# Optimization experiments

Hardware: AMD Instinct MI355X
Metric: run time of the kernel (lower is better)

## Reference

```python
import jax, jax.numpy as jnp
import numpy as np


def setup_inputs() -> dict:
    key = jax.random.key(0)
    ks = jax.random.split(key, 8)
    B, S, Ta, D = 64, 512, 8, 768
    return {
        "memory": jax.random.normal(ks[0], (B, S, D), dtype=jnp.float32),
        "aspect_states": jax.random.normal(ks[1], (B, Ta, D), dtype=jnp.float32),
        "input_ids": jnp.ones((B, S), dtype=jnp.int64),
        "input_t_ids": jnp.ones((B, Ta), dtype=jnp.int64),
        "W1": jax.random.normal(ks[2], (3 * D, D), dtype=jnp.float32) * 0.02,
        "b1": jnp.zeros((D,), dtype=jnp.float32),
        "w2": jax.random.normal(ks[3], (D,), dtype=jnp.float32) * 0.02,
        "Wm": jax.random.normal(ks[4], (D, D), dtype=jnp.float32) * 0.02,
        "bm": jnp.zeros((D,), dtype=jnp.float32),
        "Wd": jax.random.normal(ks[5], (D, 3), dtype=jnp.float32) * 0.02,
        "bd": jnp.zeros((3,), dtype=jnp.float32),
    }


def reference(memory, aspect_states, input_ids, input_t_ids, W1, b1, w2, Wm, bm, Wd, bd):
    B, S, D = memory.shape
    memory_len = jnp.sum(input_ids != 0, axis=-1)          # [B]
    aspect_len = jnp.sum(input_t_ids != 0, axis=-1)        # [B]

    # v_a: mean-pooled aspect representation  [B, D]
    v_a = jnp.sum(aspect_states, axis=1) / aspect_len.astype(memory.dtype)[:, None]
    # v_s: mean-pooled sentence representation [B, D]
    v_s = jnp.sum(memory, axis=1) / memory_len.astype(memory.dtype)[:, None]

    # locationed_memory: memory[i, idx] *= 1 - idx/memory_len[i] for idx < memory_len[i]
    idx = jnp.arange(S, dtype=memory.dtype)                 # [S]
    mlen = memory_len.astype(memory.dtype)[:, None]         # [B, 1]
    loc = jnp.where(idx[None, :] < mlen, 1.0 - idx[None, :] / mlen, 1.0)  # [B, S]
    memory = memory * loc[:, :, None]

    # chunked linear1/linear2 scorer, vectorized:
    # c_t = w2 . tanh(W1 @ [m_t ; v_a ; v_s] + b1)
    W1_m, W1_a, W1_s = W1[:D], W1[D:2 * D], W1[2 * D:]
    ctx = v_a @ W1_a + v_s @ W1_s + b1                      # [B, D]
    h = jnp.tanh(jnp.einsum("bsd,de->bse", memory, W1_m) + ctx[:, None, :])
    scores = h @ w2                                         # [B, S]
    alpha = jax.nn.softmax(scores, axis=1)

    v_ts = jnp.einsum("bsd,bs->bd", memory, alpha)          # [B, D]
    v_ns = v_ts + v_s
    v_ms = jnp.tanh(v_ns @ Wm + bm)
    logits = v_ms @ Wd + bd                                 # [B, 3]
    return logits
```

## Files before the change

### kernel.cpp

```cpp
#include <hip/hip_runtime.h>
#include <hip/hip_bf16.h>


#define NB 64
#define NS 512
#define ND 768
#define NTA 8

typedef __attribute__((ext_vector_type(8))) __bf16 bf16x8;
typedef __attribute__((ext_vector_type(4))) float f32x4;

#define OFF_SCORES 0u
#define OFF_VS 131072u
#define OFF_VTS 327680u
#define OFF_CTX 524288u
#define OFF_U 720896u
#define ZERO_BYTES 917504u
#define OFF_VA 917504u
#define OFF_LENS 1245184u
#define OFF_W1MT 1246208u
#define OFF_MP 2425856u

__device__ __forceinline__ float fast_tanh(float x) {
  x = fminf(fmaxf(x, -15.f), 15.f);
  float t = __expf(2.f * x);
  return __fdividef(t - 1.f, t + 1.f);
}

__device__ __forceinline__ unsigned bfpack2(float a, float b) {
  unsigned ua = __float_as_uint(a), ub = __float_as_uint(b);
  ua = (ua + 0x7FFFu + ((ua >> 16) & 1u)) >> 16;
  ub = (ub + 0x7FFFu + ((ub >> 16) & 1u)) >> 16;
  return ua | (ub << 16);
}

__device__ __forceinline__ unsigned short bf16b(float f) {
  unsigned u = __float_as_uint(f);
  u = (u + 0x7FFFu + ((u >> 16) & 1u)) >> 16;
  return (unsigned short)u;
}

__device__ __forceinline__ void async_copy16(const void* g, void* l) {
  __builtin_amdgcn_global_load_lds(
      (const __attribute__((address_space(1))) void*)g,
      (__attribute__((address_space(3))) void*)l, 16, 0, 0);
}

__global__ __launch_bounds__(256) void k_pre(const float* __restrict__ W1,
                                             unsigned short* __restrict__ w1mt,
                                             const int* __restrict__ ids,
                                             const int* __restrict__ tids,
                                             const float* __restrict__ aspect,
                                             float* __restrict__ v_a,
                                             float* __restrict__ lens,
                                             char* __restrict__ zws) {
  int bid = blockIdx.x, tid = threadIdx.x;
  if (bid < 576) {
    __shared__ float tile[32][33];
    int bx = bid % 24, by = bid / 24;
    int tx = tid & 31, ty = tid >> 5;
    for (int j = 0; j < 32; j += 8)
      tile[ty + j][tx] = W1[(size_t)(by * 32 + ty + j) * ND + bx * 32 + tx];
    __syncthreads();
    for (int j = 0; j < 32; j += 8)
      w1mt[(size_t)(bx * 32 + ty + j) * ND + by * 32 + tx] = bf16b(tile[tx][ty + j]);
  } else if (bid < 640) {
    int b = bid - 576;
    __shared__ int red[256];
    __shared__ float sh_inva;
    int cnt = 0;
    for (int j = tid; j < NS; j += 256) cnt += (ids[b * NS + j] != 0);
    red[tid] = cnt;
    __syncthreads();
    for (int s = 128; s > 0; s >>= 1) {
      if (tid < s) red[tid] += red[tid + s];
      __syncthreads();
    }
    if (tid == 0) {
      int mlen = red[0];
      int acnt = 0;
      for (int t = 0; t < NTA; ++t) acnt += (tids[b * NTA + t] != 0);
      lens[b] = (float)mlen;
      lens[64 + b] = 1.0f / (float)mlen;
      float inva = 1.0f / (float)acnt;
      lens[128 + b] = inva;
      sh_inva = inva;
    }
    __syncthreads();
    float inva = sh_inva;
    for (int j = tid; j < ND; j += 256) {
      float s = 0.f;
      for (int t = 0; t < NTA; ++t) s += aspect[((size_t)b * NTA + t) * ND + j];
      v_a[b * ND + j] = s * inva;
    }
  } else {
    uint4 z = {0u, 0u, 0u, 0u};
    *(uint4*)(zws + (size_t)(bid - 640) * 4096 + tid * 16) = z;
  }
}

__global__ __launch_bounds__(192) void k_vs_mprime(const float* __restrict__ memory,
                                                   const float* __restrict__ lens,
                                                   float* __restrict__ v_s,
                                                   unsigned short* __restrict__ mp) {
  int sc = blockIdx.x, b = blockIdx.y, tid = threadIdx.x;
  int d0 = tid * 4;
  float inv_mlen = lens[64 + b];
  float mlenf = lens[b];
  float s0 = 0, s1 = 0, s2 = 0, s3 = 0;
  for (int s = 0; s < 32; ++s) {
    int srow = sc * 32 + s;
    size_t row = (size_t)b * NS + srow;
    const float4 v = *(const float4*)(memory + row * ND + d0);
    s0 += v.x; s1 += v.y; s2 += v.z; s3 += v.w;
    float fs = (float)srow;
    float loc = (fs < mlenf) ? 1.0f - fs * inv_mlen : 1.0f;
    uint2 pk;
    pk.x = bfpack2(v.x * loc, v.y * loc);
    pk.y = bfpack2(v.z * loc, v.w * loc);
    *(uint2*)(mp + row * ND + d0) = pk;
  }
  float* p = v_s + b * ND + d0;
  atomicAdd(p + 0, s0 * inv_mlen);
  atomicAdd(p + 1, s1 * inv_mlen);
  atomicAdd(p + 2, s2 * inv_mlen);
  atomicAdd(p + 3, s3 * inv_mlen);
}

__global__ __launch_bounds__(256) void k_ctx(const float* __restrict__ W1,
                                             const float* __restrict__ v_a,
                                             const float* __restrict__ v_s,
                                             float* __restrict__ ctx) {
  int et = blockIdx.x, bt = blockIdx.y, dc = blockIdx.z, tid = threadIdx.x;
  __shared__ float vbuf[8][192];
  int b0 = bt * 8;
  for (int l = tid; l < 8 * 192; l += 256) {
    int bb = l / 192, jj = l % 192;
    int k = dc * 192 + jj;
    vbuf[bb][jj] = (k < ND) ? v_a[(b0 + bb) * ND + k] : v_s[(b0 + bb) * ND + (k - ND)];
  }
  __syncthreads();
  int e = et * 256 + tid;
  const float* Wk = W1 + (size_t)(ND + dc * 192) * ND + e;
  float acc[8] = {0.f, 0.f, 0.f, 0.f, 0.f, 0.f, 0.f, 0.f};
#pragma unroll 4
  for (int j = 0; j < 192; ++j) {
    float w = Wk[(size_t)j * ND];
#pragma unroll
    for (int bb = 0; bb < 8; ++bb) acc[bb] += vbuf[bb][j] * w;
  }
#pragma unroll
  for (int bb = 0; bb < 8; ++bb) atomicAdd(&ctx[(b0 + bb) * ND + e], acc[bb]);
}

__global__ __launch_bounds__(256) void k_gemm_scores(const unsigned short* __restrict__ mp,
                                                     const unsigned short* __restrict__ w1mt,
                                                     const float* __restrict__ ctx,
                                                     const float* __restrict__ b1,
                                                     const float* __restrict__ w2,
                                                     float* __restrict__ scores) {
  __shared__ char lds[32768];
  char* ldsA = lds;
  char* ldsB = lds + 16384;
  const int tid = threadIdx.x;
  const int wave = tid >> 6, lane = tid & 63;
  const int bid = blockIdx.x;
  const int xcd = bid & 7, j = bid >> 3;
  const int et = j % 6;
  const int rt = xcd * 32 + j / 6;
  const int row0 = rt * 128, n0 = et * 128;
  const int b = row0 >> 9;
  const int wm = wave & 1, wn = wave >> 1;

  const int lrow = lane >> 3;
  const int qlog = (lane & 7) ^ lrow;
  const char* Abase = (const char*)mp + (size_t)(row0 + lrow) * (ND * 2) + qlog * 16;
  const char* Bbase = (const char*)w1mt + (size_t)(n0 + lrow) * (ND * 2) + qlog * 16;

  f32x4 acc[4][4];
#pragma unroll
  for (int i = 0; i < 4; ++i)
#pragma unroll
    for (int t = 0; t < 4; ++t) acc[i][t] = (f32x4){0.f, 0.f, 0.f, 0.f};

  const int q2 = lane >> 4, c = lane & 15;
  int offA0[4], offB0[4];
#pragma unroll
  for (int i = 0; i < 4; ++i) {
    int ml = wm * 64 + i * 16 + c;
    offA0[i] = ml * 128 + ((q2 ^ (ml & 7)) * 16);
    int nl = wn * 64 + i * 16 + c;
    offB0[i] = nl * 128 + ((q2 ^ (nl & 7)) * 16);
  }

  for (int kb = 0; kb < ND * 2; kb += 128) {
#pragma unroll
    for (int i = 0; i < 4; ++i) {
      int g = wave * 4 + i;
      async_copy16(Abase + (size_t)g * 8 * (ND * 2) + kb, ldsA + g * 1024);
      async_copy16(Bbase + (size_t)g * 8 * (ND * 2) + kb, ldsB + g * 1024);
    }
    __syncthreads();
#pragma unroll
    for (int kk = 0; kk < 2; ++kk) {
      const int x = kk * 64;
      bf16x8 bfrag[4];
#pragma unroll
      for (int t = 0; t < 4; ++t) bfrag[t] = *(const bf16x8*)(ldsB + (offB0[t] ^ x));
#pragma unroll
      for (int i = 0; i < 4; ++i) {
        bf16x8 afrag = *(const bf16x8*)(ldsA + (offA0[i] ^ x));
#pragma unroll
        for (int t = 0; t < 4; ++t)
          acc[i][t] = __builtin_amdgcn_mfma_f32_16x16x32_bf16(afrag, bfrag[t], acc[i][t], 0, 0, 0);
      }
    }
    __syncthreads();
  }

  float ctxv[4], w2v[4];
#pragma unroll
  for (int t = 0; t < 4; ++t) {
    int n = n0 + wn * 64 + t * 16 + c;
    ctxv[t] = ctx[b * ND + n] + b1[n];
    w2v[t] = w2[n];
  }
#pragma unroll
  for (int i = 0; i < 4; ++i) {
#pragma unroll
    for (int r = 0; r < 4; ++r) {
      float s = 0.f;
#pragma unroll
      for (int t = 0; t < 4; ++t) s += fast_tanh(acc[i][t][r] + ctxv[t]) * w2v[t];
      s += __shfl_xor(s, 1, 64);
      s += __shfl_xor(s, 2, 64);
      s += __shfl_xor(s, 4, 64);
      s += __shfl_xor(s, 8, 64);
      if (c == 0) atomicAdd(&scores[row0 + wm * 64 + i * 16 + q2 * 4 + r], s);
    }
  }
}

__global__ __launch_bounds__(192) void k_vts_sm(const unsigned short* __restrict__ mp,
                                                const float* __restrict__ scores,
                                                float* __restrict__ v_ts) {
  int sc = blockIdx.x, b = blockIdx.y, tid = threadIdx.x;
  int wid = tid >> 6, lane = tid & 63;
  __shared__ float sm[3], ss[3];
  __shared__ float al[32];
  float v[3];
#pragma unroll
  for (int k = 0; k < 3; ++k) {
    int j = tid + k * 192;
    v[k] = (j < NS) ? scores[b * NS + j] : -1e30f;
  }
  float m = fmaxf(fmaxf(v[0], v[1]), v[2]);
  for (int off = 1; off < 64; off <<= 1) m = fmaxf(m, __shfl_xor(m, off, 64));
  if (lane == 0) sm[wid] = m;
  __syncthreads();
  float M = fmaxf(fmaxf(sm[0], sm[1]), sm[2]);
  float e = 0.f;
#pragma unroll
  for (int k = 0; k < 3; ++k)
    if (tid + k * 192 < NS) e += __expf(v[k] - M);
  for (int off = 1; off < 64; off <<= 1) e += __shfl_xor(e, off, 64);
  if (lane == 0) ss[wid] = e;
  __syncthreads();
  float invS = 1.0f / (ss[0] + ss[1] + ss[2]);
  if (tid < 32) al[tid] = __expf(scores[b * NS + sc * 32 + tid] - M) * invS;
  __syncthreads();

  int d0 = tid * 4;
  float a0 = 0, a1 = 0, a2 = 0, a3 = 0;
  for (int s = 0; s < 32; ++s) {
    size_t row = (size_t)b * NS + sc * 32 + s;
    uint2 pk = *(const uint2*)(mp + row * ND + d0);
    float a = al[s];
    a0 += a * __uint_as_float(pk.x << 16);
    a1 += a * __uint_as_float(pk.x & 0xFFFF0000u);
    a2 += a * __uint_as_float(pk.y << 16);
    a3 += a * __uint_as_float(pk.y & 0xFFFF0000u);
  }
  float* p = v_ts + b * ND + d0;
  atomicAdd(p + 0, a0);
  atomicAdd(p + 1, a1);
  atomicAdd(p + 2, a2);
  atomicAdd(p + 3, a3);
}

__global__ __launch_bounds__(256) void k_final1(const float* __restrict__ v_ts,
                                                const float* __restrict__ v_s,
                                                const float* __restrict__ Wm,
                                                float* __restrict__ u) {
  int et = blockIdx.x, bt = blockIdx.y, dc = blockIdx.z, tid = threadIdx.x;
  __shared__ float vbuf[8][192];
  int b0 = bt * 8;
  for (int l = tid; l < 8 * 192; l += 256) {
    int bb = l / 192, jj = l % 192;
    int d = dc * 192 + jj;
    vbuf[bb][jj] = v_ts[(b0 + bb) * ND + d] + v_s[(b0 + bb) * ND + d];
  }
  __syncthreads();
  int e = et * 256 + tid;
  const float* Wk = Wm + (size_t)(dc * 192) * ND + e;
  float acc[8] = {0.f, 0.f, 0.f, 0.f, 0.f, 0.f, 0.f, 0.f};
#pragma unroll 4
  for (int j = 0; j < 192; ++j) {
    float w = Wk[(size_t)j * ND];
#pragma unroll
    for (int bb = 0; bb < 8; ++bb) acc[bb] += vbuf[bb][j] * w;
  }
#pragma unroll
  for (int bb = 0; bb < 8; ++bb) atomicAdd(&u[(b0 + bb) * ND + e], acc[bb]);
}

__global__ __launch_bounds__(256) void k_final2(const float* __restrict__ u,
                                                const float* __restrict__ bm,
                                                const float* __restrict__ Wd,
                                                const float* __restrict__ bd,
                                                float* __restrict__ out) {
  int b = blockIdx.x, tid = threadIdx.x;
  int wid = tid >> 6, lane = tid & 63;
  __shared__ float red[4][3];
  float p0 = 0, p1 = 0, p2 = 0;
  for (int e = tid; e < ND; e += 256) {
    float vm = fast_tanh(u[b * ND + e] + bm[e]);
    p0 += vm * Wd[e * 3 + 0];
    p1 += vm * Wd[e * 3 + 1];
    p2 += vm * Wd[e * 3 + 2];
  }
  for (int off = 1; off < 64; off <<= 1) {
    p0 += __shfl_xor(p0, off, 64);
    p1 += __shfl_xor(p1, off, 64);
    p2 += __shfl_xor(p2, off, 64);
  }
  if (lane == 0) { red[wid][0] = p0; red[wid][1] = p1; red[wid][2] = p2; }
  __syncthreads();
  if (tid == 0) {
    out[b * 3 + 0] = red[0][0] + red[1][0] + red[2][0] + red[3][0] + bd[0];
    out[b * 3 + 1] = red[0][1] + red[1][1] + red[2][1] + red[3][1] + bd[1];
    out[b * 3 + 2] = red[0][2] + red[1][2] + red[2][2] + red[3][2] + bd[2];
  }
}

extern "C" void kernel_launch(void* const* d_in, const int* in_sizes, int n_in,
                              void* d_out, int out_size, void* d_ws, size_t ws_size,
                              hipStream_t stream) {
  const float* memory = (const float*)d_in[0];
  const float* aspect = (const float*)d_in[1];
  const int* ids = (const int*)d_in[2];
  const int* tids = (const int*)d_in[3];
  const float* W1 = (const float*)d_in[4];
  const float* b1 = (const float*)d_in[5];
  const float* w2 = (const float*)d_in[6];
  const float* Wm = (const float*)d_in[7];
  const float* bm = (const float*)d_in[8];
  const float* Wd = (const float*)d_in[9];
  const float* bd = (const float*)d_in[10];
  float* out = (float*)d_out;

  char* ws = (char*)d_ws;
  float* scores = (float*)(ws + OFF_SCORES);
  float* v_s = (float*)(ws + OFF_VS);
  float* v_ts = (float*)(ws + OFF_VTS);
  float* ctx = (float*)(ws + OFF_CTX);
  float* u = (float*)(ws + OFF_U);
  float* v_a = (float*)(ws + OFF_VA);
  float* lens = (float*)(ws + OFF_LENS);
  unsigned short* w1mt = (unsigned short*)(ws + OFF_W1MT);
  unsigned short* mp = (unsigned short*)(ws + OFF_MP);

  k_pre<<<864, 256, 0, stream>>>(W1, w1mt, ids, tids, aspect, v_a, lens, ws);
  k_vs_mprime<<<dim3(16, NB), 192, 0, stream>>>(memory, lens, v_s, mp);
  k_ctx<<<dim3(3, 8, 8), 256, 0, stream>>>(W1, v_a, v_s, ctx);
  k_gemm_scores<<<1536, 256, 0, stream>>>(mp, w1mt, ctx, b1, w2, scores);
  k_vts_sm<<<dim3(16, NB), 192, 0, stream>>>(mp, scores, v_ts);
  k_final1<<<dim3(3, 8, 4), 256, 0, stream>>>(v_ts, v_s, Wm, u);
  k_final2<<<NB, 256, 0, stream>>>(u, bm, Wd, bd, out);
}
```

Before: 324.6 us.

## Fuse all stages into one persistent cooperative kernel with grid syncs

Replaces seven separate kernel launches with a single cooperative persistent kernel that runs each former stage in a grid-stride loop, separated by grid-wide barriers. The aim is to remove per-launch overhead and the gaps between dependent kernels. The grid is sized from the occupancy query, capped at 1024 blocks. Fixed-work stages such as the GEMM now loop over fewer resident blocks, and each grid.sync adds its own barrier cost. The old multi-kernel path is kept as a fallback if the cooperative launch fails.

```diff
diff --git a/kernel.cpp b/kernel.cpp
--- a/kernel.cpp
+++ b/kernel.cpp
@@ -1,5 +1,8 @@
 #include <hip/hip_runtime.h>
 #include <hip/hip_bf16.h>
+#include <hip/hip_cooperative_groups.h>
+
+namespace cg = cooperative_groups;
 
 
 #define NB 64
@@ -44,6 +47,291 @@
   __builtin_amdgcn_global_load_lds(
       (const __attribute__((address_space(1))) void*)g,
       (__attribute__((address_space(3))) void*)l, 16, 0, 0);
+}
+
+__global__ __launch_bounds__(256, 4) void k_mega(
+    const float* __restrict__ memory, const float* __restrict__ aspect,
+    const int* __restrict__ ids, const int* __restrict__ tids,
+    const float* __restrict__ W1, const float* __restrict__ b1,
+    const float* __restrict__ w2, const float* __restrict__ Wm,
+    const float* __restrict__ bm, const float* __restrict__ Wd,
+    const float* __restrict__ bd, float* __restrict__ out,
+    float* __restrict__ scores, float* __restrict__ v_s,
+    float* __restrict__ v_ts, float* __restrict__ ctx, float* __restrict__ u,
+    float* __restrict__ v_a, float* __restrict__ lens,
+    unsigned short* __restrict__ w1mt, unsigned short* __restrict__ mp,
+    char* __restrict__ zws) {
+  cg::grid_group grid = cg::this_grid();
+  const int bid = blockIdx.x, tid = threadIdx.x;
+  const int nblk = gridDim.x;
+  __shared__ __align__(16) char smem[32768];
+
+  for (int vb = bid; vb < 864; vb += nblk) {
+    if (vb < 576) {
+      float(*tile)[33] = (float(*)[33])smem;
+      int bx = vb % 24, by = vb / 24;
+      int tx = tid & 31, ty = tid >> 5;
+      for (int j = 0; j < 32; j += 8)
+        tile[ty + j][tx] = W1[(size_t)(by * 32 + ty + j) * ND + bx * 32 + tx];
+      __syncthreads();
+      for (int j = 0; j < 32; j += 8)
+        w1mt[(size_t)(bx * 32 + ty + j) * ND + by * 32 + tx] = bf16b(tile[tx][ty + j]);
+    } else if (vb < 640) {
+      int b = vb - 576;
+      int* red = (int*)smem;
+      float* sh_inva = (float*)(smem + 1024);
+      int cnt = 0;
+      for (int j = tid; j < NS; j += 256) cnt += (ids[b * NS + j] != 0);
+      red[tid] = cnt;
+      __syncthreads();
+      for (int s = 128; s > 0; s >>= 1) {
+        if (tid < s) red[tid] += red[tid + s];
+        __syncthreads();
+      }
+      if (tid == 0) {
+        int mlen = red[0];
+        int acnt = 0;
+        for (int t = 0; t < NTA; ++t) acnt += (tids[b * NTA + t] != 0);
+        lens[b] = (float)mlen;
+        lens[64 + b] = 1.0f / (float)mlen;
+        float inva = 1.0f / (float)acnt;
+        lens[128 + b] = inva;
+        *sh_inva = inva;
+      }
+      __syncthreads();
+      float inva = *sh_inva;
+      for (int j = tid; j < ND; j += 256) {
+        float s = 0.f;
+        for (int t = 0; t < NTA; ++t) s += aspect[((size_t)b * NTA + t) * ND + j];
+        v_a[b * ND + j] = s * inva;
+      }
+    } else {
+      uint4 z = {0u, 0u, 0u, 0u};
+      *(uint4*)(zws + (size_t)(vb - 640) * 4096 + tid * 16) = z;
+    }
+    __syncthreads();
+  }
+  grid.sync();
+
+  for (int vb = bid; vb < 1024; vb += nblk) {
+    int b = vb >> 4, sc = vb & 15;
+    if (tid < 192) {
+      int d0 = tid * 4;
+      float inv_mlen = lens[64 + b];
+      float mlenf = lens[b];
+      float s0 = 0, s1 = 0, s2 = 0, s3 = 0;
+      for (int s = 0; s < 32; ++s) {
+        int srow = sc * 32 + s;
+        size_t row = (size_t)b * NS + srow;
+        const float4 v = *(const float4*)(memory + row * ND + d0);
+        s0 += v.x; s1 += v.y; s2 += v.z; s3 += v.w;
+        float fs = (float)srow;
+        float loc = (fs < mlenf) ? 1.0f - fs * inv_mlen : 1.0f;
+        uint2 pk;
+        pk.x = bfpack2(v.x * loc, v.y * loc);
+        pk.y = bfpack2(v.z * loc, v.w * loc);
+        *(uint2*)(mp + row * ND + d0) = pk;
+      }
+      float* p = v_s + b * ND + d0;
+      atomicAdd(p + 0, s0 * inv_mlen);
+      atomicAdd(p + 1, s1 * inv_mlen);
+      atomicAdd(p + 2, s2 * inv_mlen);
+      atomicAdd(p + 3, s3 * inv_mlen);
+    }
+  }
+  grid.sync();
+
+  for (int vb = bid; vb < 768; vb += nblk) {
+    int et = vb >> 8, r = vb & 255;
+    int b = r >> 2, dc = r & 3;
+    float* vbuf = (float*)smem;
+    for (int j = tid; j < 384; j += 256) {
+      int k = dc * 384 + j;
+      vbuf[j] = (k < ND) ? v_a[b * ND + k] : v_s[b * ND + (k - ND)];
+    }
+    __syncthreads();
+    int e = et * 256 + tid;
+    float acc = 0.f;
+    const float* Wk = W1 + (size_t)(ND + dc * 384) * ND + e;
+#pragma unroll 8
+    for (int j = 0; j < 384; ++j) acc += vbuf[j] * Wk[(size_t)j * ND];
+    atomicAdd(&ctx[b * ND + e], acc);
+    __syncthreads();
+  }
+  grid.sync();
+
+  {
+    char* ldsA = smem;
+    char* ldsB = smem + 16384;
+    const int wave = tid >> 6, lane = tid & 63;
+    const int wm = wave & 1, wn = wave >> 1;
+    const int lrow = lane >> 3;
+    const int qlog = (lane & 7) ^ lrow;
+    const int q2 = lane >> 4, c = lane & 15;
+
+    for (int t = bid; t < 1536; t += nblk) {
+      const int xcd = t & 7, jj = t >> 3;
+      const int et = jj % 6;
+      const int rt = xcd * 32 + jj / 6;
+      const int row0 = rt * 128, n0 = et * 128;
+      const int b = row0 >> 9;
+
+      const char* Abase = (const char*)mp + (size_t)(row0 + lrow) * (ND * 2) + qlog * 16;
+      const char* Bbase = (const char*)w1mt + (size_t)(n0 + lrow) * (ND * 2) + qlog * 16;
+
+      f32x4 acc[4][4];
+#pragma unroll
+      for (int i = 0; i < 4; ++i)
+#pragma unroll
+        for (int t2 = 0; t2 < 4; ++t2) acc[i][t2] = (f32x4){0.f, 0.f, 0.f, 0.f};
+
+      int offA0[4], offB0[4];
+#pragma unroll
+      for (int i = 0; i < 4; ++i) {
+        int ml = wm * 64 + i * 16 + c;
+        offA0[i] = ml * 128 + ((q2 ^ (ml & 7)) * 16);
+        int nl = wn * 64 + i * 16 + c;
+        offB0[i] = nl * 128 + ((q2 ^ (nl & 7)) * 16);
+      }
+
+      __syncthreads();
+      for (int kb = 0; kb < ND * 2; kb += 128) {
+#pragma unroll
+        for (int i = 0; i < 4; ++i) {
+          int g = wave * 4 + i;
+          async_copy16(Abase + (size_t)g * 8 * (ND * 2) + kb, ldsA + g * 1024);
+          async_copy16(Bbase + (size_t)g * 8 * (ND * 2) + kb, ldsB + g * 1024);
+        }
+        __syncthreads();
+#pragma unroll
+        for (int kk = 0; kk < 2; ++kk) {
+          const int x = kk * 64;
+          bf16x8 bfrag[4];
+#pragma unroll
+          for (int t2 = 0; t2 < 4; ++t2) bfrag[t2] = *(const bf16x8*)(ldsB + (offB0[t2] ^ x));
+#pragma unroll
+          for (int i = 0; i < 4; ++i) {
+            bf16x8 afrag = *(const bf16x8*)(ldsA + (offA0[i] ^ x));
+#pragma unroll
+            for (int t2 = 0; t2 < 4; ++t2)
+              acc[i][t2] = __builtin_amdgcn_mfma_f32_16x16x32_bf16(afrag, bfrag[t2], acc[i][t2], 0, 0, 0);
+          }
+        }
+        __syncthreads();
+      }
+
+      float ctxv[4], w2v[4];
+#pragma unroll
+      for (int t2 = 0; t2 < 4; ++t2) {
+        int n = n0 + wn * 64 + t2 * 16 + c;
+        ctxv[t2] = ctx[b * ND + n] + b1[n];
+        w2v[t2] = w2[n];
+      }
+#pragma unroll
+      for (int i = 0; i < 4; ++i) {
+#pragma unroll
+        for (int r = 0; r < 4; ++r) {
+          float s = 0.f;
+#pragma unroll
+          for (int t2 = 0; t2 < 4; ++t2) s += fast_tanh(acc[i][t2][r] + ctxv[t2]) * w2v[t2];
+          s += __shfl_xor(s, 1, 64);
+          s += __shfl_xor(s, 2, 64);
+          s += __shfl_xor(s, 4, 64);
+          s += __shfl_xor(s, 8, 64);
+          if (c == 0) atomicAdd(&scores[row0 + wm * 64 + i * 16 + q2 * 4 + r], s);
+        }
+      }
+    }
+  }
+  grid.sync();
+
+  for (int vb = bid; vb < 1024; vb += nblk) {
+    int b = vb >> 4, sc = vb & 15;
+    int wid = tid >> 6, lane = tid & 63;
+    float* sm = (float*)smem;
+    float* ssum = sm + 4;
+    float* al = sm + 8;
+    float v0 = scores[b * NS + tid];
+    float v1 = scores[b * NS + 256 + tid];
+    float m = fmaxf(v0, v1);
+    for (int off = 1; off < 64; off <<= 1) m = fmaxf(m, __shfl_xor(m, off, 64));
+    if (lane == 0) sm[wid] = m;
+    __syncthreads();
+    float M = fmaxf(fmaxf(sm[0], sm[1]), fmaxf(sm[2], sm[3]));
+    float e = __expf(v0 - M) + __expf(v1 - M);
+    for (int off = 1; off < 64; off <<= 1) e += __shfl_xor(e, off, 64);
+    if (lane == 0) ssum[wid] = e;
+    __syncthreads();
+    float invS = 1.0f / (ssum[0] + ssum[1] + ssum[2] + ssum[3]);
+    if (tid < 32) al[tid] = __expf(scores[b * NS + sc * 32 + tid] - M) * invS;
+    __syncthreads();
+
+    if (tid < 192) {
+      int d0 = tid * 4;
+      float a0 = 0, a1 = 0, a2 = 0, a3 = 0;
+      for (int s = 0; s < 32; ++s) {
+        size_t row = (size_t)b * NS + sc * 32 + s;
+        uint2 pk = *(const uint2*)(mp + row * ND + d0);
+        float a = al[s];
+        a0 += a * __uint_as_float(pk.x << 16);
+        a1 += a * __uint_as_float(pk.x & 0xFFFF0000u);
+        a2 += a * __uint_as_float(pk.y << 16);
+        a3 += a * __uint_as_float(pk.y & 0xFFFF0000u);
+      }
+      float* p = v_ts + b * ND + d0;
+      atomicAdd(p + 0, a0);
+      atomicAdd(p + 1, a1);
+      atomicAdd(p + 2, a2);
+      atomicAdd(p + 3, a3);
+    }
+    __syncthreads();
+  }
+  grid.sync();
+
+  for (int vb = bid; vb < 768; vb += nblk) {
+    int et = vb >> 8, r = vb & 255;
+    int b = r >> 2, dc = r & 3;
+    float* vbuf = (float*)smem;
+    for (int j = tid; j < 192; j += 256) {
+      int d = dc * 192 + j;
+      vbuf[j] = v_ts[b * ND + d] + v_s[b * ND + d];
+    }
+    __syncthreads();
+    int e = et * 256 + tid;
+    float acc = 0.f;
+    const float* Wk = Wm + (size_t)(dc * 192) * ND + e;
+#pragma unroll 8
+    for (int j = 0; j < 192; ++j) acc += vbuf[j] * Wk[(size_t)j * ND];
+    atomicAdd(&u[b * ND + e], acc);
+    __syncthreads();
+  }
+  grid.sync();
+
+  for (int vb = bid; vb < NB; vb += nblk) {
+    int b = vb;
+    int wid = tid >> 6, lane = tid & 63;
+    float* red = (float*)smem;
+    float p0 = 0, p1 = 0, p2 = 0;
+    for (int e = tid; e < ND; e += 256) {
+      float vm = fast_tanh(u[b * ND + e] + bm[e]);
+      p0 += vm * Wd[e * 3 + 0];
+      p1 += vm * Wd[e * 3 + 1];
+      p2 += vm * Wd[e * 3 + 2];
+    }
+    for (int off = 1; off < 64; off <<= 1) {
+      p0 += __shfl_xor(p0, off, 64);
+      p1 += __shfl_xor(p1, off, 64);
+      p2 += __shfl_xor(p2, off, 64);
+    }
+    if (lane == 0) { red[wid * 3 + 0] = p0; red[wid * 3 + 1] = p1; red[wid * 3 + 2] = p2; }
+    __syncthreads();
+    if (tid == 0) {
+      out[b * 3 + 0] = red[0] + red[3] + red[6] + red[9] + bd[0];
+      out[b * 3 + 1] = red[1] + red[4] + red[7] + red[10] + bd[1];
+      out[b * 3 + 2] = red[2] + red[5] + red[8] + red[11] + bd[2];
+    }
+    __syncthreads();
+  }
 }
 
 __global__ __launch_bounds__(256) void k_pre(const float* __restrict__ W1,
@@ -171,7 +459,6 @@
   const int row0 = rt * 128, n0 = et * 128;
   const int b = row0 >> 9;
   const int wm = wave & 1, wn = wave >> 1;
-
   const int lrow = lane >> 3;
   const int qlog = (lane & 7) ^ lrow;
   const char* Abase = (const char*)mp + (size_t)(row0 + lrow) * (ND * 2) + qlog * 16;
@@ -370,11 +657,32 @@
   unsigned short* w1mt = (unsigned short*)(ws + OFF_W1MT);
   unsigned short* mp = (unsigned short*)(ws + OFF_MP);
 
-  k_pre<<<864, 256, 0, stream>>>(W1, w1mt, ids, tids, aspect, v_a, lens, ws);
-  k_vs_mprime<<<dim3(16, NB), 192, 0, stream>>>(memory, lens, v_s, mp);
-  k_ctx<<<dim3(3, 8, 8), 256, 0, stream>>>(W1, v_a, v_s, ctx);
-  k_gemm_scores<<<1536, 256, 0, stream>>>(mp, w1mt, ctx, b1, w2, scores);
-  k_vts_sm<<<dim3(16, NB), 192, 0, stream>>>(mp, scores, v_ts);
-  k_final1<<<dim3(3, 8, 4), 256, 0, stream>>>(v_ts, v_s, Wm, u);
-  k_final2<<<NB, 256, 0, stream>>>(u, bm, Wd, bd, out);
-}
+  int nb_per_cu = 0;
+  hipError_t qe = hipOccupancyMaxActiveBlocksPerMultiprocessor(&nb_per_cu, k_mega, 256, 0);
+  int grid = 0;
+  if (qe == hipSuccess && nb_per_cu > 0) {
+    grid = nb_per_cu * 256;
+    if (grid > 1024) grid = 1024;
+  }
+
+  hipError_t err = hipErrorUnknown;
+  if (grid >= 64) {
+    void* args[] = {(void*)&memory, (void*)&aspect, (void*)&ids, (void*)&tids,
+                    (void*)&W1,     (void*)&b1,     (void*)&w2,  (void*)&Wm,
+                    (void*)&bm,     (void*)&Wd,     (void*)&bd,  (void*)&out,
+                    (void*)&scores, (void*)&v_s,    (void*)&v_ts, (void*)&ctx,
+                    (void*)&u,      (void*)&v_a,    (void*)&lens, (void*)&w1mt,
+                    (void*)&mp,     (void*)&ws};
+    err = hipLaunchCooperativeKernel((void*)k_mega, dim3(grid), dim3(256), args, 0, stream);
+  }
+  if (err != hipSuccess) {
+    (void)hipGetLastError();
+    k_pre<<<864, 256, 0, stream>>>(W1, w1mt, ids, tids, aspect, v_a, lens, ws);
+    k_vs_mprime<<<dim3(16, NB), 192, 0, stream>>>(memory, lens, v_s, mp);
+    k_ctx<<<dim3(3, 8, 8), 256, 0, stream>>>(W1, v_a, v_s, ctx);
+    k_gemm_scores<<<1536, 256, 0, stream>>>(mp, w1mt, ctx, b1, w2, scores);
+    k_vts_sm<<<dim3(16, NB), 192, 0, stream>>>(mp, scores, v_ts);
+    k_final1<<<dim3(3, 8, 4), 256, 0, stream>>>(v_ts, v_s, Wm, u);
+    k_final2<<<NB, 256, 0, stream>>>(u, bm, Wd, bd, out);
+  }
+}
```

Result: slower. 667.0 us (+105.5%).
